# Performance work log

Measured on AMD Instinct MI355X. Metric: run time of the kernel, lower is better.

The kernel has to match this reference:

```python
import jax, jax.numpy as jnp
import numpy as np

EPS = 1e-5

def _bn(z, gamma, beta):
    mu = z.mean(axis=0)
    var = z.var(axis=0)  # biased, matches torch BN normalization
    return (z - mu) * jax.lax.rsqrt(var + EPS) * gamma + beta

def _sage_bn_relu(h, src, dst, n_nodes, Wl, bl, Wr, gamma, beta):
    # SAGEConv (mean aggr): out = lin_l(mean_{j in N(i)} h_j) + lin_r(h_i)
    msg = h[src]                                               # [E, d] gather
    agg = jax.ops.segment_sum(msg, dst, num_segments=n_nodes)  # [N, d]
    cnt = jax.ops.segment_sum(jnp.ones((src.shape[0], 1), h.dtype), dst,
                              num_segments=n_nodes)            # [N, 1]
    agg = jnp.where(cnt > 0, agg / jnp.maximum(cnt, 1.0), 0.0)
    out = agg @ Wl.T + bl + h @ Wr.T
    return jax.nn.relu(_bn(out, gamma, beta))

def setup_inputs() -> dict:
    key = jax.random.key(0)
    N, E, d, out_c, L, U = 50000, 800000, 128, 128, 3, 256
    ks = jax.random.split(key, 16)
    s = 1.0 / np.sqrt(d)
    return {
        "x": jax.random.normal(ks[0], (N, d), jnp.float32),
        "edge_index": jax.random.randint(ks[1], (2, E), 0, N, jnp.int64),
        "atom_mask": jax.random.uniform(ks[2], (N, 1), jnp.float32),
        "u_index": jax.random.randint(ks[3], (U,), 0, N, jnp.int64),
        "lin_l_w": jax.random.uniform(ks[4], (L, d, d), jnp.float32, -s, s),
        "lin_l_b": jax.random.uniform(ks[5], (L, d), jnp.float32, -s, s),
        "lin_r_w": jax.random.uniform(ks[6], (L, d, d), jnp.float32, -s, s),
        "bn_gamma": jnp.ones((L, d), jnp.float32),
        "bn_beta": jnp.zeros((L, d), jnp.float32),
        "ro_w1": jax.random.uniform(ks[7], (d, d), jnp.float32, -s, s),
        "ro_b1": jax.random.uniform(ks[8], (d,), jnp.float32, -s, s),
        "ro_bn_gamma": jnp.ones((d,), jnp.float32),
        "ro_bn_beta": jnp.zeros((d,), jnp.float32),
        "ro_w2": jax.random.uniform(ks[9], (out_c, d), jnp.float32, -s, s),
        "ro_b2": jax.random.uniform(ks[10], (out_c,), jnp.float32, -s, s),
    }

def reference(x, edge_index, atom_mask, u_index, lin_l_w, lin_l_b, lin_r_w,
              bn_gamma, bn_beta, ro_w1, ro_b1, ro_bn_gamma, ro_bn_beta,
              ro_w2, ro_b2):
    N = x.shape[0]
    src, dst = edge_index[0], edge_index[1]
    h = x
    for l in range(lin_l_w.shape[0]):
        h = _sage_bn_relu(h, src, dst, N, lin_l_w[l], lin_l_b[l],
                          lin_r_w[l], bn_gamma[l], bn_beta[l])
    state = h[u_index]                                         # [U, d]
    z = jax.nn.relu(_bn(h @ ro_w1.T + ro_b1, ro_bn_gamma, ro_bn_beta))
    atom = (z @ ro_w2.T + ro_b2) * atom_mask                   # [N, out]
    return (h, atom, state)
```

## Files before the change

### kernel.cpp

```cpp
#include <hip/hip_runtime.h>

#define D 128
#define LDA 136

typedef __attribute__((ext_vector_type(8))) short bf16x8;
typedef __attribute__((ext_vector_type(4))) float f32x4;

__device__ __forceinline__ ushort f2b(float f) {
  union { float f; unsigned u; } a; a.f = f;
  unsigned u = a.u;
  return (ushort)((u + 0x7fffu + ((u >> 16) & 1u)) >> 16);
}
__device__ __forceinline__ float b2f_lo(unsigned v) {
  union { unsigned u; float f; } a; a.u = v << 16; return a.f;
}
__device__ __forceinline__ float b2f_hi(unsigned v) {
  union { unsigned u; float f; } a; a.u = v & 0xffff0000u; return a.f;
}

__global__ void k_cast_pad(const float* __restrict__ s, ushort* __restrict__ d, int n4, int np4) {
  int i = blockIdx.x * blockDim.x + threadIdx.x;
  if (i >= np4) return;
  uint2 pk;
  if (i < n4) {
    float4 v = *(const float4*)&s[i * 4];
    pk.x = (unsigned)f2b(v.x) | ((unsigned)f2b(v.y) << 16);
    pk.y = (unsigned)f2b(v.z) | ((unsigned)f2b(v.w) << 16);
  } else {
    pk = make_uint2(0u, 0u);
  }
  *(uint2*)&d[i * 4] = pk;
}

__global__ void k_castw(const float* __restrict__ wl, const float* __restrict__ wr,
                        const float* __restrict__ w1, const float* __restrict__ w2,
                        ushort* __restrict__ dst, int LDD) {
  int i = blockIdx.x * blockDim.x + threadIdx.x;
  int total = 2 * LDD + 2 * D * D;
  if (i >= total) return;
  float v;
  if (i < LDD) v = wl[i];
  else if (i < 2 * LDD) v = wr[i - LDD];
  else if (i < 2 * LDD + D * D) v = w1[i - 2 * LDD];
  else v = w2[i - 2 * LDD - D * D];
  dst[i] = f2b(v);
}

__global__ void k_histrank(const int* __restrict__ dstI, int* __restrict__ cnt,
                           int* __restrict__ rankdst, int E) {
  int e = blockIdx.x * blockDim.x + threadIdx.x;
  if (e < E) {
    int d = dstI[e];
    int r = atomicAdd(&cnt[d], 1);
    rankdst[e] = (r << 16) | d;
  }
}
__global__ void k_scan1(const int* __restrict__ cnt, int* __restrict__ off,
                        int* __restrict__ bsum, int n) {
  __shared__ int sd[256];
  int t = threadIdx.x;
  int i = blockIdx.x * 256 + t;
  int x = (i < n) ? cnt[i] : 0;
  sd[t] = x;
  __syncthreads();
  for (int s = 1; s < 256; s <<= 1) {
    int v = (t >= s) ? sd[t - s] : 0;
    __syncthreads();
    sd[t] += v;
    __syncthreads();
  }
  if (i < n) off[i] = sd[t] - x;
  if (t == 255) bsum[blockIdx.x] = sd[255];
}
__global__ void k_scan2(const int* __restrict__ bsum, int* __restrict__ boff, int nb) {
  __shared__ int sd[256];
  int t = threadIdx.x;
  int x = (t < nb) ? bsum[t] : 0;
  sd[t] = x;
  __syncthreads();
  for (int s = 1; s < 256; s <<= 1) {
    int v = (t >= s) ? sd[t - s] : 0;
    __syncthreads();
    sd[t] += v;
    __syncthreads();
  }
  if (t < nb) boff[t] = sd[t] - x;
}
__global__ void k_scan3(int* __restrict__ off, const int* __restrict__ boff, int n) {
  int i = blockIdx.x * blockDim.x + threadIdx.x;
  if (i < n) off[i] += boff[i >> 8];
}
__global__ void k_fill(const int* __restrict__ srcI, const int* __restrict__ rankdst,
                       const int* __restrict__ off, int* __restrict__ eidx, int E) {
  int e = blockIdx.x * blockDim.x + threadIdx.x;
  if (e < E) {
    int rd = rankdst[e];
    int d = rd & 0xFFFF;
    eidx[off[d] + (rd >> 16)] = srcI[e];
  }
}

#define ACC8(V, B)                                        \
  a[B + 0] += b2f_lo(V.x); a[B + 1] += b2f_hi(V.x);       \
  a[B + 2] += b2f_lo(V.y); a[B + 3] += b2f_hi(V.y);       \
  a[B + 4] += b2f_lo(V.z); a[B + 5] += b2f_hi(V.z);       \
  a[B + 6] += b2f_lo(V.w); a[B + 7] += b2f_hi(V.w);

template <bool AGG>
__global__ __launch_bounds__(512) void k_fused(
    const ushort* __restrict__ hin, const ushort* __restrict__ Wl,
    const ushort* __restrict__ Wr, const float* __restrict__ bias,
    const int* __restrict__ off, const int* __restrict__ eidx,
    ushort* __restrict__ pre, float* __restrict__ sums, int N, int E) {
  __shared__ ushort aggS[128 * LDA];
  __shared__ float ls[2 * D];
  int t = threadIdx.x;
  int r0 = blockIdx.x * 128;

  if (t < 2 * D) ls[t] = 0.f;

  if (AGG) {
    int lrow = t >> 2;
    int row = r0 + lrow;
    int part = (t & 3) << 5;
    float a[32];
#pragma unroll
    for (int i = 0; i < 32; ++i) a[i] = 0.f;
    int start = 0, end = 0;
    if (row < N) { start = off[row]; end = (row == N - 1) ? E : off[row + 1]; }
    const ushort* hbase = hin + part;
#pragma unroll 2
    for (int e = start; e < end; ++e) {
      int sn = eidx[e];
      const uint4* p = (const uint4*)(hbase + (size_t)sn * D);
      uint4 v0 = p[0], v1 = p[1], v2 = p[2], v3 = p[3];
      ACC8(v0, 0) ACC8(v1, 8) ACC8(v2, 16) ACC8(v3, 24)
    }
    float inv = (end > start) ? 1.0f / (float)(end - start) : 0.f;
    unsigned o[16];
#pragma unroll
    for (int i = 0; i < 16; ++i)
      o[i] = (unsigned)f2b(a[2 * i] * inv) | ((unsigned)f2b(a[2 * i + 1] * inv) << 16);
    uint4* dst = (uint4*)&aggS[lrow * LDA + part];
    dst[0] = make_uint4(o[0], o[1], o[2], o[3]);
    dst[1] = make_uint4(o[4], o[5], o[6], o[7]);
    dst[2] = make_uint4(o[8], o[9], o[10], o[11]);
    dst[3] = make_uint4(o[12], o[13], o[14], o[15]);
  }
  __syncthreads();

  int lane = t & 63;
  int wid = t >> 6;
  int wr = wid >> 1, wc = wid & 1;
  int rw = wr * 32, cw = wc * 64;
  int lr = lane & 15, lk = (lane >> 4) * 8;

  f32x4 acc[2][4];
#pragma unroll
  for (int i = 0; i < 2; ++i)
#pragma unroll
    for (int j = 0; j < 4; ++j) acc[i][j] = (f32x4){0.f, 0.f, 0.f, 0.f};

#pragma unroll
  for (int ks = 0; ks < 4; ++ks) {
    int kb = ks * 32 + lk;
    bf16x8 aA[2], aB[2];
#pragma unroll
    for (int rt = 0; rt < 2; ++rt) {
      if (AGG) {
        aA[rt] = *(const bf16x8*)&aggS[(rw + rt * 16 + lr) * LDA + kb];
        aB[rt] = *(const bf16x8*)&hin[(size_t)(r0 + rw + rt * 16 + lr) * D + kb];
      } else {
        aA[rt] = *(const bf16x8*)&hin[(size_t)(r0 + rw + rt * 16 + lr) * D + kb];
      }
    }
#pragma unroll
    for (int jt = 0; jt < 4; ++jt) {
      bf16x8 b1 = *(const bf16x8*)&Wl[(size_t)(cw + jt * 16 + lr) * D + kb];
      acc[0][jt] = __builtin_amdgcn_mfma_f32_16x16x32_bf16(aA[0], b1, acc[0][jt], 0, 0, 0);
      acc[1][jt] = __builtin_amdgcn_mfma_f32_16x16x32_bf16(aA[1], b1, acc[1][jt], 0, 0, 0);
      if (AGG) {
        bf16x8 b2 = *(const bf16x8*)&Wr[(size_t)(cw + jt * 16 + lr) * D + kb];
        acc[0][jt] = __builtin_amdgcn_mfma_f32_16x16x32_bf16(aB[0], b2, acc[0][jt], 0, 0, 0);
        acc[1][jt] = __builtin_amdgcn_mfma_f32_16x16x32_bf16(aB[1], b2, acc[1][jt], 0, 0, 0);
      }
    }
  }

  int crow = (lane >> 4) * 4;
#pragma unroll
  for (int jt = 0; jt < 4; ++jt) {
    int col = cw + jt * 16 + lr;
    float bv = bias[col];
    float s1 = 0.f, s2 = 0.f;
#pragma unroll
    for (int rt = 0; rt < 2; ++rt) {
      int rbase = r0 + rw + rt * 16 + crow;
#pragma unroll
      for (int rg = 0; rg < 4; ++rg) {
        int row = rbase + rg;
        if (row < N) {
          float v = acc[rt][jt][rg] + bv;
          pre[(size_t)row * D + col] = f2b(v);
          s1 += v; s2 += v * v;
        }
      }
    }
    s1 += __shfl_xor(s1, 16, 64); s1 += __shfl_xor(s1, 32, 64);
    s2 += __shfl_xor(s2, 16, 64); s2 += __shfl_xor(s2, 32, 64);
    if (lane < 16) {
      atomicAdd(&ls[cw + jt * 16 + lane], s1);
      atomicAdd(&ls[D + cw + jt * 16 + lane], s2);
    }
  }
  __syncthreads();
  if (t < 2 * D) atomicAdd(&sums[t], ls[t]);
}

template <bool F32OUT>
__global__ void k_bnrelu(const ushort* __restrict__ pre, const float* __restrict__ sums,
                         const float* __restrict__ gamma, const float* __restrict__ beta,
                         float* __restrict__ fout, ushort* __restrict__ bout,
                         int N, int Np, float invN) {
  int i4 = blockIdx.x * blockDim.x + threadIdx.x;
  if (i4 >= Np * (D / 4)) return;
  int row = i4 >> 5;
  int c4 = (i4 & 31) * 4;
  uint2 pk;
  if (row < N) {
    uint2 pv = *(const uint2*)&pre[(size_t)row * D + c4];
    float4 v = make_float4(b2f_lo(pv.x), b2f_hi(pv.x), b2f_lo(pv.y), b2f_hi(pv.y));
    float4 s = *(const float4*)&sums[c4];
    float4 q = *(const float4*)&sums[D + c4];
    float4 g = *(const float4*)&gamma[c4];
    float4 b = *(const float4*)&beta[c4];
    float mu, var, sc, sh;
    mu = s.x * invN; var = fmaxf(q.x * invN - mu * mu, 0.f);
    sc = g.x * rsqrtf(var + 1e-5f); sh = b.x - mu * sc;
    v.x = fmaxf(fmaf(v.x, sc, sh), 0.f);
    mu = s.y * invN; var = fmaxf(q.y * invN - mu * mu, 0.f);
    sc = g.y * rsqrtf(var + 1e-5f); sh = b.y - mu * sc;
    v.y = fmaxf(fmaf(v.y, sc, sh), 0.f);
    mu = s.z * invN; var = fmaxf(q.z * invN - mu * mu, 0.f);
    sc = g.z * rsqrtf(var + 1e-5f); sh = b.z - mu * sc;
    v.z = fmaxf(fmaf(v.z, sc, sh), 0.f);
    mu = s.w * invN; var = fmaxf(q.w * invN - mu * mu, 0.f);
    sc = g.w * rsqrtf(var + 1e-5f); sh = b.w - mu * sc;
    v.w = fmaxf(fmaf(v.w, sc, sh), 0.f);
    if (F32OUT) *(float4*)&fout[(size_t)row * D + c4] = v;
    pk.x = (unsigned)f2b(v.x) | ((unsigned)f2b(v.y) << 16);
    pk.y = (unsigned)f2b(v.z) | ((unsigned)f2b(v.w) << 16);
  } else {
    pk = make_uint2(0u, 0u);
  }
  *(uint2*)&bout[(size_t)row * D + c4] = pk;
}

__global__ __launch_bounds__(256) void k_mmfin(
    const ushort* __restrict__ A, const ushort* __restrict__ W,
    const float* __restrict__ bias, const float* __restrict__ mask,
    float* __restrict__ out, int N) {
  int t = threadIdx.x;
  int lane = t & 63;
  int wid = t >> 6;
  int wr = wid >> 1, wc = wid & 1;
  int r0 = blockIdx.x * 128 + wr * 64;
  int c0 = wc * 64;
  int lr = lane & 15, lk = (lane >> 4) * 8;

  f32x4 acc[4][4];
#pragma unroll
  for (int i = 0; i < 4; ++i)
#pragma unroll
    for (int j = 0; j < 4; ++j) acc[i][j] = (f32x4){0.f, 0.f, 0.f, 0.f};

#pragma unroll
  for (int ks = 0; ks < 4; ++ks) {
    int kb = ks * 32 + lk;
    bf16x8 a1[4];
#pragma unroll
    for (int rt = 0; rt < 4; ++rt)
      a1[rt] = *(const bf16x8*)&A[(size_t)(r0 + rt * 16 + lr) * D + kb];
#pragma unroll
    for (int jt = 0; jt < 4; ++jt) {
      bf16x8 b1 = *(const bf16x8*)&W[(size_t)(c0 + jt * 16 + lr) * D + kb];
#pragma unroll
      for (int rt = 0; rt < 4; ++rt)
        acc[rt][jt] = __builtin_amdgcn_mfma_f32_16x16x32_bf16(a1[rt], b1, acc[rt][jt], 0, 0, 0);
    }
  }

  int crow = (lane >> 4) * 4;
#pragma unroll
  for (int rt = 0; rt < 4; ++rt) {
    int rbase = r0 + rt * 16 + crow;
#pragma unroll
    for (int jt = 0; jt < 4; ++jt) {
      int col = c0 + jt * 16 + lr;
      float bv = bias[col];
#pragma unroll
      for (int rg = 0; rg < 4; ++rg) {
        int row = rbase + rg;
        if (row < N) {
          float m = mask[row];
          out[(size_t)row * D + col] = (acc[rt][jt][rg] + bv) * m;
        }
      }
    }
  }
}

__global__ void k_gather(const float* __restrict__ h, const int* __restrict__ uidx,
                         float* __restrict__ outp, int U) {
  int u = blockIdx.x;
  int t = threadIdx.x;
  int s = uidx[u];
  *(float4*)&outp[(size_t)u * D + t * 4] = *(const float4*)&h[(size_t)s * D + t * 4];
}

extern "C" void kernel_launch(void* const* d_in, const int* in_sizes, int n_in,
                              void* d_out, int out_size, void* d_ws, size_t ws_size,
                              hipStream_t stream) {
  const float* x        = (const float*)d_in[0];
  const int*   edge     = (const int*)d_in[1];
  const float* amask    = (const float*)d_in[2];
  const int*   uindex   = (const int*)d_in[3];
  const float* lin_l_w  = (const float*)d_in[4];
  const float* lin_l_b  = (const float*)d_in[5];
  const float* lin_r_w  = (const float*)d_in[6];
  const float* bn_gamma = (const float*)d_in[7];
  const float* bn_beta  = (const float*)d_in[8];
  const float* ro_w1    = (const float*)d_in[9];
  const float* ro_b1    = (const float*)d_in[10];
  const float* ro_bng   = (const float*)d_in[11];
  const float* ro_bnb   = (const float*)d_in[12];
  const float* ro_w2    = (const float*)d_in[13];
  const float* ro_b2    = (const float*)d_in[14];

  const int N = in_sizes[0] / D;
  const int E = in_sizes[1] / 2;
  const int U = in_sizes[3];
  const int L = in_sizes[4] / (D * D);
  const int Np = ((N + 127) / 128) * 128;
  const int LDD = L * D * D;

  const int* srcI = edge;
  const int* dstI = edge + E;

  float* outH     = (float*)d_out;
  float* outAtom  = outH + (size_t)N * D;
  float* outState = outAtom + (size_t)N * D;

  char* w = (char*)d_ws;
  ushort* hb   = (ushort*)w; w += (size_t)Np * D * 2;
  ushort* pre  = (ushort*)w; w += (size_t)Np * D * 2;
  ushort* wall = (ushort*)w; w += (size_t)(2 * LDD + 2 * D * D) * 2;
  int*    cnt  = (int*)w;    w += (size_t)N * 4;
  float*  sums = (float*)w;  w += 4 * 2 * D * 4;
  int* off     = (int*)w;    w += (size_t)N * 4;
  int* rankdst = (int*)w;    w += (size_t)E * 4;
  int* eidx    = (int*)w;    w += (size_t)E * 4;
  int* bsum    = (int*)w;    w += 1024;
  int* boff    = (int*)w;    w += 1024;

  ushort* wlb = wall;
  ushort* wrb = wlb + (size_t)LDD;
  ushort* w1b = wrb + (size_t)LDD;
  ushort* w2b = w1b + (size_t)D * D;

  k_cast_pad<<<(Np * D / 4 + 255) / 256, 256, 0, stream>>>(x, hb, N * D / 4, Np * D / 4);
  k_castw<<<(2 * LDD + 2 * D * D + 255) / 256, 256, 0, stream>>>(lin_l_w, lin_r_w, ro_w1, ro_w2, wall, LDD);
  hipMemsetAsync(cnt, 0, (size_t)N * 4 + 4 * 2 * D * 4, stream);

  int nbE = (E + 255) / 256;
  int nbN = (N + 255) / 256;
  k_histrank<<<nbE, 256, 0, stream>>>(dstI, cnt, rankdst, E);
  k_scan1<<<nbN, 256, 0, stream>>>(cnt, off, bsum, N);
  k_scan2<<<1, 256, 0, stream>>>(bsum, boff, nbN);
  k_scan3<<<nbN, 256, 0, stream>>>(off, boff, N);
  k_fill<<<nbE, 256, 0, stream>>>(srcI, rankdst, off, eidx, E);

  const int mmBlocks = Np / 128;
  const int bnBlocks = (Np * (D / 4) + 255) / 256;
  const float invN = 1.0f / (float)N;

  for (int l = 0; l < L; ++l) {
    float* lsums = sums + (size_t)l * 2 * D;
    k_fused<true><<<mmBlocks, 512, 0, stream>>>(
        hb, wlb + (size_t)l * D * D, wrb + (size_t)l * D * D,
        lin_l_b + (size_t)l * D, off, eidx, pre, lsums, N, E);
    if (l == L - 1)
      k_bnrelu<true><<<bnBlocks, 256, 0, stream>>>(pre, lsums, bn_gamma + (size_t)l * D,
                                                   bn_beta + (size_t)l * D, outH, hb, N, Np, invN);
    else
      k_bnrelu<false><<<bnBlocks, 256, 0, stream>>>(pre, lsums, bn_gamma + (size_t)l * D,
                                                    bn_beta + (size_t)l * D, nullptr, hb, N, Np, invN);
  }

  float* rsums = sums + (size_t)L * 2 * D;
  k_fused<false><<<mmBlocks, 512, 0, stream>>>(
      hb, w1b, nullptr, ro_b1, off, eidx, pre, rsums, N, E);
  k_bnrelu<false><<<bnBlocks, 256, 0, stream>>>(pre, rsums, ro_bng, ro_bnb, nullptr, hb, N, Np, invN);
  k_mmfin<<<mmBlocks, 256, 0, stream>>>(hb, w2b, ro_b2, amask, outAtom, N);
  k_gather<<<U, 32, 0, stream>>>(outH, uindex, outState, U);
}
```

Before: 328.7 us.

## Halve fused block size and split neighbor gather into two concurrent edge streams

The fused aggregation+GEMM kernel now handles 64 rows per 256-thread block instead of 128 rows per 512 threads, doubling the block count. Each thread's neighbor-mean loop now walks two halves of its edge list at once into separate accumulators, so two independent row gathers are in flight per iteration instead of one. This targets gather latency and load imbalance across high-degree rows. It doubles the accumulator registers per thread, which may reduce occupancy, and each block now reloads the weight tiles for half as many rows.

```diff
diff --git a/kernel.cpp b/kernel.cpp
--- a/kernel.cpp
+++ b/kernel.cpp
@@ -100,47 +100,60 @@
   }
 }
 
-#define ACC8(V, B)                                        \
-  a[B + 0] += b2f_lo(V.x); a[B + 1] += b2f_hi(V.x);       \
-  a[B + 2] += b2f_lo(V.y); a[B + 3] += b2f_hi(V.y);       \
-  a[B + 4] += b2f_lo(V.z); a[B + 5] += b2f_hi(V.z);       \
-  a[B + 6] += b2f_lo(V.w); a[B + 7] += b2f_hi(V.w);
+#define ACC8(A, V, B)                                             \
+  A[B + 0] += b2f_lo(V.x); A[B + 1] += b2f_hi(V.x);               \
+  A[B + 2] += b2f_lo(V.y); A[B + 3] += b2f_hi(V.y);               \
+  A[B + 4] += b2f_lo(V.z); A[B + 5] += b2f_hi(V.z);               \
+  A[B + 6] += b2f_lo(V.w); A[B + 7] += b2f_hi(V.w);
 
 template <bool AGG>
-__global__ __launch_bounds__(512) void k_fused(
+__global__ __launch_bounds__(256) void k_fused(
     const ushort* __restrict__ hin, const ushort* __restrict__ Wl,
     const ushort* __restrict__ Wr, const float* __restrict__ bias,
     const int* __restrict__ off, const int* __restrict__ eidx,
     ushort* __restrict__ pre, float* __restrict__ sums, int N, int E) {
-  __shared__ ushort aggS[128 * LDA];
+  __shared__ ushort aggS[64 * LDA];
   __shared__ float ls[2 * D];
   int t = threadIdx.x;
-  int r0 = blockIdx.x * 128;
-
-  if (t < 2 * D) ls[t] = 0.f;
+  int r0 = blockIdx.x * 64;
+
+  ls[t] = 0.f;
 
   if (AGG) {
     int lrow = t >> 2;
     int row = r0 + lrow;
     int part = (t & 3) << 5;
-    float a[32];
-#pragma unroll
-    for (int i = 0; i < 32; ++i) a[i] = 0.f;
+    float a0[32], a1[32];
+#pragma unroll
+    for (int i = 0; i < 32; ++i) { a0[i] = 0.f; a1[i] = 0.f; }
     int start = 0, end = 0;
     if (row < N) { start = off[row]; end = (row == N - 1) ? E : off[row + 1]; }
+    int deg = end - start;
+    int mid = start + (deg >> 1);
     const ushort* hbase = hin + part;
-#pragma unroll 2
-    for (int e = start; e < end; ++e) {
-      int sn = eidx[e];
-      const uint4* p = (const uint4*)(hbase + (size_t)sn * D);
-      uint4 v0 = p[0], v1 = p[1], v2 = p[2], v3 = p[3];
-      ACC8(v0, 0) ACC8(v1, 8) ACC8(v2, 16) ACC8(v3, 24)
-    }
-    float inv = (end > start) ? 1.0f / (float)(end - start) : 0.f;
+    int e0 = start, e1 = mid;
+    for (; e0 < mid; ++e0, ++e1) {
+      int s0 = eidx[e0];
+      int s1 = eidx[e1];
+      const uint4* p0 = (const uint4*)(hbase + (size_t)s0 * D);
+      const uint4* p1 = (const uint4*)(hbase + (size_t)s1 * D);
+      uint4 u0 = p0[0], u1 = p0[1], u2 = p0[2], u3 = p0[3];
+      uint4 w0 = p1[0], w1 = p1[1], w2 = p1[2], w3 = p1[3];
+      ACC8(a0, u0, 0) ACC8(a0, u1, 8) ACC8(a0, u2, 16) ACC8(a0, u3, 24)
+      ACC8(a1, w0, 0) ACC8(a1, w1, 8) ACC8(a1, w2, 16) ACC8(a1, w3, 24)
+    }
+    for (; e1 < end; ++e1) {
+      int s1 = eidx[e1];
+      const uint4* p1 = (const uint4*)(hbase + (size_t)s1 * D);
+      uint4 w0 = p1[0], w1 = p1[1], w2 = p1[2], w3 = p1[3];
+      ACC8(a1, w0, 0) ACC8(a1, w1, 8) ACC8(a1, w2, 16) ACC8(a1, w3, 24)
+    }
+    float inv = (deg > 0) ? 1.0f / (float)deg : 0.f;
     unsigned o[16];
 #pragma unroll
     for (int i = 0; i < 16; ++i)
-      o[i] = (unsigned)f2b(a[2 * i] * inv) | ((unsigned)f2b(a[2 * i + 1] * inv) << 16);
+      o[i] = (unsigned)f2b((a0[2 * i] + a1[2 * i]) * inv) |
+             ((unsigned)f2b((a0[2 * i + 1] + a1[2 * i + 1]) * inv) << 16);
     uint4* dst = (uint4*)&aggS[lrow * LDA + part];
     dst[0] = make_uint4(o[0], o[1], o[2], o[3]);
     dst[1] = make_uint4(o[4], o[5], o[6], o[7]);
@@ -214,7 +227,7 @@
     }
   }
   __syncthreads();
-  if (t < 2 * D) atomicAdd(&sums[t], ls[t]);
+  atomicAdd(&sums[t], ls[t]);
 }
 
 template <bool F32OUT>
@@ -380,13 +393,13 @@
   k_scan3<<<nbN, 256, 0, stream>>>(off, boff, N);
   k_fill<<<nbE, 256, 0, stream>>>(srcI, rankdst, off, eidx, E);
 
-  const int mmBlocks = Np / 128;
+  const int fusedBlocks = Np / 64;
   const int bnBlocks = (Np * (D / 4) + 255) / 256;
   const float invN = 1.0f / (float)N;
 
   for (int l = 0; l < L; ++l) {
     float* lsums = sums + (size_t)l * 2 * D;
-    k_fused<true><<<mmBlocks, 512, 0, stream>>>(
+    k_fused<true><<<fusedBlocks, 256, 0, stream>>>(
         hb, wlb + (size_t)l * D * D, wrb + (size_t)l * D * D,
         lin_l_b + (size_t)l * D, off, eidx, pre, lsums, N, E);
     if (l == L - 1)
@@ -398,9 +411,9 @@
   }
 
   float* rsums = sums + (size_t)L * 2 * D;
-  k_fused<false><<<mmBlocks, 512, 0, stream>>>(
+  k_fused<false><<<fusedBlocks, 256, 0, stream>>>(
       hb, w1b, nullptr, ro_b1, off, eidx, pre, rsums, N, E);
   k_bnrelu<false><<<bnBlocks, 256, 0, stream>>>(pre, rsums, ro_bng, ro_bnb, nullptr, hb, N, Np, invN);
-  k_mmfin<<<mmBlocks, 256, 0, stream>>>(hb, w2b, ro_b2, amask, outAtom, N);
+  k_mmfin<<<Np / 128, 256, 0, stream>>>(hb, w2b, ro_b2, amask, outAtom, N);
   k_gather<<<U, 32, 0, stream>>>(outH, uindex, outState, U);
 }
```

After: 384.7 us. 17.1% more time.

## Defer BatchNorm+ReLU into next layer's gather and GEMM loads, shrink edge indices

Applied to the files above, without the earlier changes.

Removes the intermediate bnrelu kernels between SAGE layers. Each fused layer now computes BN scale/shift from the previous layer's sums and applies normalize+ReLU while gathering neighbor rows and loading self rows. The readout final matmul does the same for the readout BN. Edge source indices are stored as 16-bit values, which halves gather index traffic, and the cast/weight/memset prep launches are merged into one kernel. The trade-off is recomputing the affine+ReLU once per edge visit instead of once per node. The 16-bit indices also silently truncate sources when N exceeds 65535.

```diff
diff --git a/kernel.cpp b/kernel.cpp
--- a/kernel.cpp
+++ b/kernel.cpp
@@ -18,32 +18,37 @@
   union { unsigned u; float f; } a; a.u = v & 0xffff0000u; return a.f;
 }
 
-__global__ void k_cast_pad(const float* __restrict__ s, ushort* __restrict__ d, int n4, int np4) {
+__global__ void k_prep(const float* __restrict__ x, const float* __restrict__ wl,
+                       const float* __restrict__ wr, const float* __restrict__ w1,
+                       const float* __restrict__ w2, ushort* __restrict__ hb,
+                       ushort* __restrict__ wall, uint4* __restrict__ zr,
+                       int nX4, int npX4, int LDD, int nZero4) {
   int i = blockIdx.x * blockDim.x + threadIdx.x;
-  if (i >= np4) return;
-  uint2 pk;
-  if (i < n4) {
-    float4 v = *(const float4*)&s[i * 4];
-    pk.x = (unsigned)f2b(v.x) | ((unsigned)f2b(v.y) << 16);
-    pk.y = (unsigned)f2b(v.z) | ((unsigned)f2b(v.w) << 16);
-  } else {
-    pk = make_uint2(0u, 0u);
-  }
-  *(uint2*)&d[i * 4] = pk;
-}
-
-__global__ void k_castw(const float* __restrict__ wl, const float* __restrict__ wr,
-                        const float* __restrict__ w1, const float* __restrict__ w2,
-                        ushort* __restrict__ dst, int LDD) {
-  int i = blockIdx.x * blockDim.x + threadIdx.x;
-  int total = 2 * LDD + 2 * D * D;
-  if (i >= total) return;
-  float v;
-  if (i < LDD) v = wl[i];
-  else if (i < 2 * LDD) v = wr[i - LDD];
-  else if (i < 2 * LDD + D * D) v = w1[i - 2 * LDD];
-  else v = w2[i - 2 * LDD - D * D];
-  dst[i] = f2b(v);
+  if (i < npX4) {
+    uint2 pk;
+    if (i < nX4) {
+      float4 v = *(const float4*)&x[i * 4];
+      pk.x = (unsigned)f2b(v.x) | ((unsigned)f2b(v.y) << 16);
+      pk.y = (unsigned)f2b(v.z) | ((unsigned)f2b(v.w) << 16);
+    } else {
+      pk = make_uint2(0u, 0u);
+    }
+    *(uint2*)&hb[i * 4] = pk;
+    return;
+  }
+  int j = i - npX4;
+  int W = 2 * LDD + 2 * D * D;
+  if (j < W) {
+    float v;
+    if (j < LDD) v = wl[j];
+    else if (j < 2 * LDD) v = wr[j - LDD];
+    else if (j < 2 * LDD + D * D) v = w1[j - 2 * LDD];
+    else v = w2[j - 2 * LDD - D * D];
+    wall[j] = f2b(v);
+    return;
+  }
+  int z = j - W;
+  if (z < nZero4) zr[z] = make_uint4(0u, 0u, 0u, 0u);
 }
 
 __global__ void k_histrank(const int* __restrict__ dstI, int* __restrict__ cnt,
@@ -91,41 +96,90 @@
   if (i < n) off[i] += boff[i >> 8];
 }
 __global__ void k_fill(const int* __restrict__ srcI, const int* __restrict__ rankdst,
-                       const int* __restrict__ off, int* __restrict__ eidx, int E) {
+                       const int* __restrict__ off, ushort* __restrict__ eidx, int E) {
   int e = blockIdx.x * blockDim.x + threadIdx.x;
   if (e < E) {
     int rd = rankdst[e];
     int d = rd & 0xFFFF;
-    eidx[off[d] + (rd >> 16)] = srcI[e];
-  }
-}
-
-#define ACC8(V, B)                                        \
-  a[B + 0] += b2f_lo(V.x); a[B + 1] += b2f_hi(V.x);       \
-  a[B + 2] += b2f_lo(V.y); a[B + 3] += b2f_hi(V.y);       \
-  a[B + 4] += b2f_lo(V.z); a[B + 5] += b2f_hi(V.z);       \
-  a[B + 6] += b2f_lo(V.w); a[B + 7] += b2f_hi(V.w);
-
-template <bool AGG>
+    eidx[off[d] + (rd >> 16)] = (ushort)srcI[e];
+  }
+}
+
+#define PROC8(V, B)                                                              \
+  {                                                                              \
+    float x_;                                                                    \
+    x_ = b2f_lo(V.x); if (DEFER) x_ = fmaxf(fmaf(x_, sc[B+0], sh[B+0]), 0.f);    \
+    a[B+0] += x_;                                                                \
+    x_ = b2f_hi(V.x); if (DEFER) x_ = fmaxf(fmaf(x_, sc[B+1], sh[B+1]), 0.f);    \
+    a[B+1] += x_;                                                                \
+    x_ = b2f_lo(V.y); if (DEFER) x_ = fmaxf(fmaf(x_, sc[B+2], sh[B+2]), 0.f);    \
+    a[B+2] += x_;                                                                \
+    x_ = b2f_hi(V.y); if (DEFER) x_ = fmaxf(fmaf(x_, sc[B+3], sh[B+3]), 0.f);    \
+    a[B+3] += x_;                                                                \
+    x_ = b2f_lo(V.z); if (DEFER) x_ = fmaxf(fmaf(x_, sc[B+4], sh[B+4]), 0.f);    \
+    a[B+4] += x_;                                                                \
+    x_ = b2f_hi(V.z); if (DEFER) x_ = fmaxf(fmaf(x_, sc[B+5], sh[B+5]), 0.f);    \
+    a[B+5] += x_;                                                                \
+    x_ = b2f_lo(V.w); if (DEFER) x_ = fmaxf(fmaf(x_, sc[B+6], sh[B+6]), 0.f);    \
+    a[B+6] += x_;                                                                \
+    x_ = b2f_hi(V.w); if (DEFER) x_ = fmaxf(fmaf(x_, sc[B+7], sh[B+7]), 0.f);    \
+    a[B+7] += x_;                                                                \
+  }
+
+template <bool DEFER>
+__device__ __forceinline__ bf16x8 loadBfrag(const ushort* __restrict__ p,
+                                            const float* __restrict__ scshS, int kb) {
+  bf16x8 f = *(const bf16x8*)p;
+  if (DEFER) {
+#pragma unroll
+    for (int q = 0; q < 8; ++q) {
+      float x = b2f_lo((unsigned)(ushort)f[q]);
+      x = fmaxf(fmaf(x, scshS[kb + q], scshS[D + kb + q]), 0.f);
+      f[q] = (short)f2b(x);
+    }
+  }
+  return f;
+}
+
+template <bool AGG, bool DEFER>
 __global__ __launch_bounds__(512) void k_fused(
-    const ushort* __restrict__ hin, const ushort* __restrict__ Wl,
-    const ushort* __restrict__ Wr, const float* __restrict__ bias,
-    const int* __restrict__ off, const int* __restrict__ eidx,
-    ushort* __restrict__ pre, float* __restrict__ sums, int N, int E) {
+    const ushort* __restrict__ hin, const float* __restrict__ psums,
+    const float* __restrict__ pgamma, const float* __restrict__ pbeta,
+    const ushort* __restrict__ Wl, const ushort* __restrict__ Wr,
+    const float* __restrict__ bias, const int* __restrict__ off,
+    const ushort* __restrict__ eidx, ushort* __restrict__ pre,
+    float* __restrict__ sums, int N, int E, float invN) {
   __shared__ ushort aggS[128 * LDA];
   __shared__ float ls[2 * D];
+  __shared__ float scshS[2 * D];
   int t = threadIdx.x;
   int r0 = blockIdx.x * 128;
 
   if (t < 2 * D) ls[t] = 0.f;
+
+  if (DEFER) {
+    if (t < D) {
+      float mu = psums[t] * invN;
+      float var = fmaxf(psums[D + t] * invN - mu * mu, 0.f);
+      float s = pgamma[t] * rsqrtf(var + 1e-5f);
+      scshS[t] = s;
+      scshS[D + t] = pbeta[t] - mu * s;
+    }
+    __syncthreads();
+  }
 
   if (AGG) {
     int lrow = t >> 2;
     int row = r0 + lrow;
     int part = (t & 3) << 5;
     float a[32];
+    float sc[32], sh[32];
 #pragma unroll
     for (int i = 0; i < 32; ++i) a[i] = 0.f;
+    if (DEFER) {
+#pragma unroll
+      for (int i = 0; i < 32; ++i) { sc[i] = scshS[part + i]; sh[i] = scshS[D + part + i]; }
+    }
     int start = 0, end = 0;
     if (row < N) { start = off[row]; end = (row == N - 1) ? E : off[row + 1]; }
     const ushort* hbase = hin + part;
@@ -134,9 +188,10 @@
       int sn = eidx[e];
       const uint4* p = (const uint4*)(hbase + (size_t)sn * D);
       uint4 v0 = p[0], v1 = p[1], v2 = p[2], v3 = p[3];
-      ACC8(v0, 0) ACC8(v1, 8) ACC8(v2, 16) ACC8(v3, 24)
-    }
-    float inv = (end > start) ? 1.0f / (float)(end - start) : 0.f;
+      PROC8(v0, 0) PROC8(v1, 8) PROC8(v2, 16) PROC8(v3, 24)
+    }
+    int deg = end - start;
+    float inv = (deg > 0) ? 1.0f / (float)deg : 0.f;
     unsigned o[16];
 #pragma unroll
     for (int i = 0; i < 16; ++i)
@@ -169,7 +224,7 @@
     for (int rt = 0; rt < 2; ++rt) {
       if (AGG) {
         aA[rt] = *(const bf16x8*)&aggS[(rw + rt * 16 + lr) * LDA + kb];
-        aB[rt] = *(const bf16x8*)&hin[(size_t)(r0 + rw + rt * 16 + lr) * D + kb];
+        aB[rt] = loadBfrag<DEFER>(&hin[(size_t)(r0 + rw + rt * 16 + lr) * D + kb], scshS, kb);
       } else {
         aA[rt] = *(const bf16x8*)&hin[(size_t)(r0 + rw + rt * 16 + lr) * D + kb];
       }
@@ -217,7 +272,6 @@
   if (t < 2 * D) atomicAdd(&sums[t], ls[t]);
 }
 
-template <bool F32OUT>
 __global__ void k_bnrelu(const ushort* __restrict__ pre, const float* __restrict__ sums,
                          const float* __restrict__ gamma, const float* __restrict__ beta,
                          float* __restrict__ fout, ushort* __restrict__ bout,
@@ -247,7 +301,7 @@
     mu = s.w * invN; var = fmaxf(q.w * invN - mu * mu, 0.f);
     sc = g.w * rsqrtf(var + 1e-5f); sh = b.w - mu * sc;
     v.w = fmaxf(fmaf(v.w, sc, sh), 0.f);
-    if (F32OUT) *(float4*)&fout[(size_t)row * D + c4] = v;
+    *(float4*)&fout[(size_t)row * D + c4] = v;
     pk.x = (unsigned)f2b(v.x) | ((unsigned)f2b(v.y) << 16);
     pk.y = (unsigned)f2b(v.z) | ((unsigned)f2b(v.w) << 16);
   } else {
@@ -257,10 +311,21 @@
 }
 
 __global__ __launch_bounds__(256) void k_mmfin(
-    const ushort* __restrict__ A, const ushort* __restrict__ W,
-    const float* __restrict__ bias, const float* __restrict__ mask,
-    float* __restrict__ out, int N) {
+    const ushort* __restrict__ A, const float* __restrict__ psums,
+    const float* __restrict__ pgamma, const float* __restrict__ pbeta,
+    const ushort* __restrict__ W, const float* __restrict__ bias,
+    const float* __restrict__ mask, float* __restrict__ out, int N, float invN) {
+  __shared__ float scshS[2 * D];
   int t = threadIdx.x;
+  if (t < D) {
+    float mu = psums[t] * invN;
+    float var = fmaxf(psums[D + t] * invN - mu * mu, 0.f);
+    float s = pgamma[t] * rsqrtf(var + 1e-5f);
+    scshS[t] = s;
+    scshS[D + t] = pbeta[t] - mu * s;
+  }
+  __syncthreads();
+
   int lane = t & 63;
   int wid = t >> 6;
   int wr = wid >> 1, wc = wid & 1;
@@ -280,7 +345,7 @@
     bf16x8 a1[4];
 #pragma unroll
     for (int rt = 0; rt < 4; ++rt)
-      a1[rt] = *(const bf16x8*)&A[(size_t)(r0 + rt * 16 + lr) * D + kb];
+      a1[rt] = loadBfrag<true>(&A[(size_t)(r0 + rt * 16 + lr) * D + kb], scshS, kb);
 #pragma unroll
     for (int jt = 0; jt < 4; ++jt) {
       bf16x8 b1 = *(const bf16x8*)&W[(size_t)(c0 + jt * 16 + lr) * D + kb];
@@ -353,13 +418,14 @@
 
   char* w = (char*)d_ws;
   ushort* hb   = (ushort*)w; w += (size_t)Np * D * 2;
-  ushort* pre  = (ushort*)w; w += (size_t)Np * D * 2;
+  ushort* preA = (ushort*)w; w += (size_t)Np * D * 2;
+  ushort* preB = (ushort*)w; w += (size_t)Np * D * 2;
   ushort* wall = (ushort*)w; w += (size_t)(2 * LDD + 2 * D * D) * 2;
   int*    cnt  = (int*)w;    w += (size_t)N * 4;
   float*  sums = (float*)w;  w += 4 * 2 * D * 4;
   int* off     = (int*)w;    w += (size_t)N * 4;
   int* rankdst = (int*)w;    w += (size_t)E * 4;
-  int* eidx    = (int*)w;    w += (size_t)E * 4;
+  ushort* eidx = (ushort*)w; w += (size_t)((E + 1) & ~1) * 2;
   int* bsum    = (int*)w;    w += 1024;
   int* boff    = (int*)w;    w += 1024;
 
@@ -368,9 +434,16 @@
   ushort* w1b = wrb + (size_t)LDD;
   ushort* w2b = w1b + (size_t)D * D;
 
-  k_cast_pad<<<(Np * D / 4 + 255) / 256, 256, 0, stream>>>(x, hb, N * D / 4, Np * D / 4);
-  k_castw<<<(2 * LDD + 2 * D * D + 255) / 256, 256, 0, stream>>>(lin_l_w, lin_r_w, ro_w1, ro_w2, wall, LDD);
-  hipMemsetAsync(cnt, 0, (size_t)N * 4 + 4 * 2 * D * 4, stream);
+  const float invN = 1.0f / (float)N;
+
+  {
+    int nX4 = N * D / 4, npX4 = Np * D / 4;
+    int W = 2 * LDD + 2 * D * D;
+    int nZero4 = (N + 4 * 2 * D) / 4;
+    int total = npX4 + W + nZero4;
+    k_prep<<<(total + 255) / 256, 256, 0, stream>>>(x, lin_l_w, lin_r_w, ro_w1, ro_w2,
+                                                    hb, wall, (uint4*)cnt, nX4, npX4, LDD, nZero4);
+  }
 
   int nbE = (E + 255) / 256;
   int nbN = (N + 255) / 256;
@@ -380,27 +453,26 @@
   k_scan3<<<nbN, 256, 0, stream>>>(off, boff, N);
   k_fill<<<nbE, 256, 0, stream>>>(srcI, rankdst, off, eidx, E);
 
-  const int mmBlocks = Np / 128;
+  const int fusedBlocks = Np / 128;
   const int bnBlocks = (Np * (D / 4) + 255) / 256;
-  const float invN = 1.0f / (float)N;
-
-  for (int l = 0; l < L; ++l) {
-    float* lsums = sums + (size_t)l * 2 * D;
-    k_fused<true><<<mmBlocks, 512, 0, stream>>>(
-        hb, wlb + (size_t)l * D * D, wrb + (size_t)l * D * D,
-        lin_l_b + (size_t)l * D, off, eidx, pre, lsums, N, E);
-    if (l == L - 1)
-      k_bnrelu<true><<<bnBlocks, 256, 0, stream>>>(pre, lsums, bn_gamma + (size_t)l * D,
-                                                   bn_beta + (size_t)l * D, outH, hb, N, Np, invN);
-    else
-      k_bnrelu<false><<<bnBlocks, 256, 0, stream>>>(pre, lsums, bn_gamma + (size_t)l * D,
-                                                    bn_beta + (size_t)l * D, nullptr, hb, N, Np, invN);
-  }
-
-  float* rsums = sums + (size_t)L * 2 * D;
-  k_fused<false><<<mmBlocks, 512, 0, stream>>>(
-      hb, w1b, nullptr, ro_b1, off, eidx, pre, rsums, N, E);
-  k_bnrelu<false><<<bnBlocks, 256, 0, stream>>>(pre, rsums, ro_bng, ro_bnb, nullptr, hb, N, Np, invN);
-  k_mmfin<<<mmBlocks, 256, 0, stream>>>(hb, w2b, ro_b2, amask, outAtom, N);
+
+  k_fused<true, false><<<fusedBlocks, 512, 0, stream>>>(
+      hb, nullptr, nullptr, nullptr, wlb, wrb, lin_l_b,
+      off, eidx, preA, sums, N, E, invN);
+  k_fused<true, true><<<fusedBlocks, 512, 0, stream>>>(
+      preA, sums, bn_gamma, bn_beta, wlb + (size_t)D * D, wrb + (size_t)D * D,
+      lin_l_b + D, off, eidx, preB, sums + 2 * D, N, E, invN);
+  k_fused<true, true><<<fusedBlocks, 512, 0, stream>>>(
+      preB, sums + 2 * D, bn_gamma + D, bn_beta + D, wlb + (size_t)2 * D * D,
+      wrb + (size_t)2 * D * D, lin_l_b + 2 * D, off, eidx, preA, sums + 4 * D, N, E, invN);
+
+  k_bnrelu<<<bnBlocks, 256, 0, stream>>>(preA, sums + 4 * D, bn_gamma + 2 * D,
+                                         bn_beta + 2 * D, outH, hb, N, Np, invN);
+
+  k_fused<false, false><<<fusedBlocks, 512, 0, stream>>>(
+      hb, nullptr, nullptr, nullptr, w1b, nullptr, ro_b1,
+      off, eidx, preB, sums + 6 * D, N, E, invN);
+  k_mmfin<<<Np / 128, 256, 0, stream>>>(preB, sums + 6 * D, ro_bng, ro_bnb,
+                                        w2b, ro_b2, amask, outAtom, N, invN);
   k_gather<<<U, 32, 0, stream>>>(outH, uindex, outState, U);
 }
```

New measurement: 333.5 us. No clear change (+1.5%).
